# Performance work log

Measured on AMD Instinct MI355X. Metric: run time of the kernel, lower is better.

The kernel has to match this reference:

```python
import jax, jax.numpy as jnp
import numpy as np

N = 100000
D = 256
E = 300000


def setup_inputs() -> dict:
    key = jax.random.key(0)
    ks = jax.random.split(key, 9)
    x_all = jax.random.normal(ks[0], (N, D), dtype=jnp.float32)
    edge_index = jax.random.randint(ks[1], (2, E), 0, N, dtype=jnp.int64)
    s = 1.0 / np.sqrt(D)
    params = {}
    for i, layer in enumerate(["1", "2", "3"]):
        params[f"Wl{layer}"] = jax.random.uniform(ks[2 + 2 * i], (D, D), jnp.float32, -s, s)
        params[f"Wr{layer}"] = jax.random.uniform(ks[3 + 2 * i], (D, D), jnp.float32, -s, s)
        params[f"b{layer}"] = jnp.zeros((D,), jnp.float32)
    return {"edge_index": edge_index, "x_all": x_all, **params}


def sage_conv(x, src, dst, Wl, Wr, b):
    # PyG SAGEConv: lin_l(mean_{j in N(i)} x_j) + lin_r(x_i), bias on lin_l
    msgs = x[src]                                        # [E, D] gather
    agg = jax.ops.segment_sum(msgs, dst, num_segments=N)  # [N, D]
    deg = jax.ops.segment_sum(jnp.ones((src.shape[0],), x.dtype), dst, num_segments=N)
    agg = agg / jnp.maximum(deg, 1.0)[:, None]           # mean; isolated nodes -> 0
    return agg @ Wl.T + x @ Wr.T + b


def reference(edge_index, x_all, Wl1, Wr1, b1, Wl2, Wr2, b2, Wl3, Wr3, b3):
    src, dst = edge_index[0], edge_index[1]
    x = jax.nn.relu(sage_conv(x_all, src, dst, Wl1, Wr1, b1))
    # dropout p=0.4 is identity at inference (training=False)
    x = jax.nn.relu(sage_conv(x, src, dst, Wl2, Wr2, b2))
    x = sage_conv(x, src, dst, Wl3, Wr3, b3)
    return x
```

## Files before the change

### kernel.cpp

```cpp
#include <hip/hip_runtime.h>

typedef unsigned short ushort_t;
typedef unsigned int   u32;
typedef __attribute__((ext_vector_type(8))) short bf16x8;
typedef __attribute__((ext_vector_type(4))) float f32x4;

#define NNODES 100000
#define DIM    256
#define NEDGE  300000
#define KSTEPS 16
#define BROWS  64
#define SLICE  16384
#define MFMA16 __builtin_amdgcn_mfma_f32_16x16x32_bf16


__global__ void count_kernel(const int* __restrict__ dst, int* __restrict__ cnt, int E) {
    int e = blockIdx.x * blockDim.x + threadIdx.x;
    if (e < E) atomicAdd(&cnt[dst[e]], 1);
}

__global__ void scan1(const int* __restrict__ cnt, int* __restrict__ partial, int n) {
    __shared__ int s[256];
    int i = blockIdx.x * 256 + threadIdx.x;
    s[threadIdx.x] = (i < n) ? cnt[i] : 0;
    __syncthreads();
    for (int off = 128; off > 0; off >>= 1) {
        if (threadIdx.x < off) s[threadIdx.x] += s[threadIdx.x + off];
        __syncthreads();
    }
    if (threadIdx.x == 0) partial[blockIdx.x] = s[0];
}

__global__ void scan2(int* __restrict__ partial, int nb) {
    __shared__ int s[512];
    int t = threadIdx.x;
    int orig = (t < nb) ? partial[t] : 0;
    s[t] = orig;
    __syncthreads();
    for (int off = 1; off < 512; off <<= 1) {
        int v = (t >= off) ? s[t - off] : 0;
        __syncthreads();
        s[t] += v;
        __syncthreads();
    }
    if (t < nb) partial[t] = s[t] - orig;
}

__global__ void scan3(const int* __restrict__ cnt, const int* __restrict__ partial,
                      int* __restrict__ row_start, int n) {
    __shared__ int s[256];
    int i = blockIdx.x * 256 + threadIdx.x;
    int v = (i < n) ? cnt[i] : 0;
    s[threadIdx.x] = v;
    __syncthreads();
    for (int off = 1; off < 256; off <<= 1) {
        int t = (threadIdx.x >= off) ? s[threadIdx.x - off] : 0;
        __syncthreads();
        s[threadIdx.x] += t;
        __syncthreads();
    }
    if (i < n) row_start[i] = partial[blockIdx.x] + s[threadIdx.x] - v;
}

__global__ void fill_csr(const int* __restrict__ src, const int* __restrict__ dst,
                         const int* __restrict__ row_start, int* __restrict__ cursor,
                         int* __restrict__ esrc, int E) {
    int e = blockIdx.x * blockDim.x + threadIdx.x;
    if (e < E) {
        int d = dst[e];
        int pos = row_start[d] + atomicAdd(&cursor[d], 1);
        esrc[pos] = src[e];
    }
}


__device__ __forceinline__ float bfhi(unsigned u) { return __uint_as_float(u << 16); }
__device__ __forceinline__ float bflo(unsigned u) { return __uint_as_float(u & 0xFFFF0000u); }

__device__ __forceinline__ void split4pack(float v0, float v1, float v2, float v3,
                                           uint2& hi, uint2& lo) {
    unsigned u0 = __float_as_uint(v0), u1 = __float_as_uint(v1);
    unsigned u2 = __float_as_uint(v2), u3 = __float_as_uint(v3);
    hi.x = (u0 >> 16) | (u1 & 0xFFFF0000u);
    hi.y = (u2 >> 16) | (u3 & 0xFFFF0000u);
    unsigned w0 = __float_as_uint(v0 - bflo(u0)), w1 = __float_as_uint(v1 - bflo(u1));
    unsigned w2 = __float_as_uint(v2 - bflo(u2)), w3 = __float_as_uint(v3 - bflo(u3));
    lo.x = (w0 >> 16) | (w1 & 0xFFFF0000u);
    lo.y = (w2 >> 16) | (w3 & 0xFFFF0000u);
}

__global__ __launch_bounds__(256) void split_x(const float* __restrict__ x,
                                               ushort_t* __restrict__ x2) {
    int idx = blockIdx.x * 256 + threadIdx.x;
    if (idx >= NNODES * 64) return;
    int node = idx >> 6, lane = idx & 63;
    float4 v = ((const float4*)(x + (size_t)node * DIM))[lane];
    uint2 hi, lo;
    split4pack(v.x, v.y, v.z, v.w, hi, lo);
    *(uint2*)(x2 + (size_t)node * 512 + lane * 4)       = hi;
    *(uint2*)(x2 + (size_t)node * 512 + 256 + lane * 4) = lo;
}

__global__ __launch_bounds__(256) void aggregate2(
    const int* __restrict__ esrc, const int* __restrict__ row_start,
    const int* __restrict__ cnt, const ushort_t* __restrict__ x2,
    ushort_t* __restrict__ agg2)
{
    int node = (blockIdx.x * blockDim.x + threadIdx.x) >> 6;
    int lane = threadIdx.x & 63;
    if (node >= NNODES) return;
    int start = row_start[node];
    int c = cnt[node];
    float a0 = 0.f, a1 = 0.f, a2 = 0.f, a3 = 0.f;
    for (int i = 0; i < c; i++) {
        int s = esrc[start + i];
        const uint2 h = *(const uint2*)(x2 + (size_t)s * 512 + lane * 4);
        const uint2 l = *(const uint2*)(x2 + (size_t)s * 512 + 256 + lane * 4);
        a0 += bfhi(h.x) + bfhi(l.x);
        a1 += bflo(h.x) + bflo(l.x);
        a2 += bfhi(h.y) + bfhi(l.y);
        a3 += bflo(h.y) + bflo(l.y);
    }
    float inv = (c > 0) ? 1.0f / (float)c : 0.0f;
    uint2 hi, lo;
    split4pack(a0 * inv, a1 * inv, a2 * inv, a3 * inv, hi, lo);
    *(uint2*)(agg2 + (size_t)node * 512 + lane * 4)       = hi;
    *(uint2*)(agg2 + (size_t)node * 512 + 256 + lane * 4) = lo;
}

__global__ void conv_weights(const float* __restrict__ Wl, const float* __restrict__ Wr,
                             ushort_t* __restrict__ Bsw) {
    int idx = blockIdx.x * 256 + threadIdx.x;
    if (idx >= 256 * 512) return;
    int n = idx >> 9, k = idx & 511;
    float v = (k < DIM) ? Wl[n * DIM + k] : Wr[n * DIM + (k - DIM)];
    unsigned u = __float_as_uint(v);
    float lo = v - bflo(u);
    int ks = k >> 5, q = (k >> 3) & 3, j = k & 7;
    int ct = n >> 4, nn = n & 15;
    int base = ks * SLICE + ct * 512 + q * 128 + nn * 8 + j;
    Bsw[base]        = (ushort_t)(u >> 16);
    Bsw[base + 8192] = (ushort_t)(__float_as_uint(lo) >> 16);
}

__global__ __launch_bounds__(256, 4) void sage_gemm_mfma(
    const ushort_t* __restrict__ agg2, const ushort_t* __restrict__ xin2,
    const ushort_t* __restrict__ Bsw, const float* __restrict__ bias,
    void* __restrict__ outp, int M, int out_split)
{
    const int tid  = threadIdx.x;
    const int lane = tid & 63;
    const int cg   = tid >> 6;
    const int lrow = lane & 15;
    const int quad = lane >> 4;

    const int rowbase = blockIdx.x * BROWS;
    int r[4];
    #pragma unroll
    for (int rt = 0; rt < 4; rt++)
        r[rt] = min(rowbase + rt * 16 + lrow, M - 1);
    const int kq = quad * 8;
    const int ctbase = cg * 4;

    f32x4 acc[4][4];
    #pragma unroll
    for (int i = 0; i < 4; i++)
        #pragma unroll
        for (int j = 0; j < 4; j++)
            acc[i][j] = (f32x4){0.f, 0.f, 0.f, 0.f};

    #pragma unroll
    for (int ks = 0; ks < KSTEPS; ks++) {
        const ushort_t* ab = (ks < 8) ? agg2 : xin2;
        const int kk = (ks & 7) * 32 + kq;

        bf16x8 fh[4], fl[4];
        #pragma unroll
        for (int rt = 0; rt < 4; rt++) {
            const ushort_t* p = ab + (size_t)r[rt] * 512 + kk;
            fh[rt] = *(const bf16x8*)(p);
            fl[rt] = *(const bf16x8*)(p + 256);
        }

        const ushort_t* bp = Bsw + (size_t)ks * SLICE + ctbase * 512 + lane * 8;

        __builtin_amdgcn_s_setprio(1);
        #pragma unroll
        for (int ct = 0; ct < 4; ct++) {
            const bf16x8 bh = *(const bf16x8*)(bp + ct * 512);
            const bf16x8 bl = *(const bf16x8*)(bp + 8192 + ct * 512);
            #pragma unroll
            for (int rt = 0; rt < 4; rt++) {
                acc[rt][ct] = MFMA16(fh[rt], bh, acc[rt][ct], 0, 0, 0);
                acc[rt][ct] = MFMA16(fl[rt], bh, acc[rt][ct], 0, 0, 0);
                acc[rt][ct] = MFMA16(fh[rt], bl, acc[rt][ct], 0, 0, 0);
            }
        }
        __builtin_amdgcn_s_setprio(0);
    }

    __syncthreads();

    #pragma unroll
    for (int ct = 0; ct < 4; ct++) {
        const int col = (ctbase + ct) * 16 + lrow;
        const float bv = bias[col];
        #pragma unroll
        for (int rt = 0; rt < 4; rt++) {
            const int row = rowbase + rt * 16 + quad * 4;
            #pragma unroll
            for (int rr = 0; rr < 4; rr++) {
                if (row + rr < M) {
                    float v = acc[rt][ct][rr] + bv;
                    if (out_split) {
                        v = fmaxf(v, 0.f);
                        unsigned u = __float_as_uint(v);
                        float lo = v - bflo(u);
                        ushort_t* o = (ushort_t*)outp + (size_t)(row + rr) * 512 + col;
                        o[0]   = (ushort_t)(u >> 16);
                        o[256] = (ushort_t)(__float_as_uint(lo) >> 16);
                    } else {
                        ((float*)outp)[(size_t)(row + rr) * DIM + col] = v;
                    }
                }
            }
        }
    }
}

extern "C" void kernel_launch(void* const* d_in, const int* in_sizes, int n_in,
                              void* d_out, int out_size, void* d_ws, size_t ws_size,
                              hipStream_t stream) {
    const int*   edge = (const int*)d_in[0];
    const int*   src  = edge;
    const int*   dst  = edge + NEDGE;
    const float* x    = (const float*)d_in[1];
    const float* Wl1  = (const float*)d_in[2];
    const float* Wr1  = (const float*)d_in[3];
    const float* b1   = (const float*)d_in[4];
    const float* Wl2  = (const float*)d_in[5];
    const float* Wr2  = (const float*)d_in[6];
    const float* b2   = (const float*)d_in[7];
    const float* Wl3  = (const float*)d_in[8];
    const float* Wr3  = (const float*)d_in[9];
    const float* b3   = (const float*)d_in[10];

    ushort_t* agg2      = (ushort_t*)d_ws;
    int*      cnt       = (int*)(agg2 + (size_t)NNODES * 512);
    int*      row_start = cnt + NNODES;
    int*      cursor    = row_start + NNODES;
    int*      partial   = cursor + NNODES;
    int*      esrc      = partial + 512;
    ushort_t* Bsw       = (ushort_t*)(esrc + NEDGE);

    ushort_t* x2 = (ushort_t*)d_out;

    const int nScanBlocks = (NNODES + 255) / 256;

    hipMemsetAsync(cnt, 0, NNODES * sizeof(int), stream);
    hipMemsetAsync(cursor, 0, NNODES * sizeof(int), stream);
    count_kernel<<<(NEDGE + 255) / 256, 256, 0, stream>>>(dst, cnt, NEDGE);
    scan1<<<nScanBlocks, 256, 0, stream>>>(cnt, partial, NNODES);
    scan2<<<1, 512, 0, stream>>>(partial, nScanBlocks);
    scan3<<<nScanBlocks, 256, 0, stream>>>(cnt, partial, row_start, NNODES);
    fill_csr<<<(NEDGE + 255) / 256, 256, 0, stream>>>(src, dst, row_start, cursor, esrc, NEDGE);

    split_x<<<(NNODES * 64 + 255) / 256, 256, 0, stream>>>(x, x2);

    const int aggBlocks  = (NNODES * 64 + 255) / 256;
    const int gemmBlocks = (NNODES + BROWS - 1) / BROWS;
    const int convBlocks = (256 * 512 + 255) / 256;

    conv_weights<<<convBlocks, 256, 0, stream>>>(Wl1, Wr1, Bsw);
    aggregate2<<<aggBlocks, 256, 0, stream>>>(esrc, row_start, cnt, x2, agg2);
    sage_gemm_mfma<<<gemmBlocks, 256, 0, stream>>>(agg2, x2, Bsw, b1, (void*)x2, NNODES, 1);

    conv_weights<<<convBlocks, 256, 0, stream>>>(Wl2, Wr2, Bsw);
    aggregate2<<<aggBlocks, 256, 0, stream>>>(esrc, row_start, cnt, x2, agg2);
    sage_gemm_mfma<<<gemmBlocks, 256, 0, stream>>>(agg2, x2, Bsw, b2, (void*)x2, NNODES, 1);

    conv_weights<<<convBlocks, 256, 0, stream>>>(Wl3, Wr3, Bsw);
    aggregate2<<<aggBlocks, 256, 0, stream>>>(esrc, row_start, cnt, x2, agg2);
    sage_gemm_mfma<<<gemmBlocks, 256, 0, stream>>>(agg2, x2, Bsw, b3, d_out, NNODES, 0);
}
```

Before: 760.9 us.

## Stage weight column slice in LDS and split GEMM across column blocks

The GEMM is restructured so each 512-thread block covers 512 rows and one 64-column slice of the output. That slice's weight panel (64K bf16 halves) is loaded into LDS once per block via global_load_lds, instead of every wave reading B from global memory each k-step. A-fragments are double-buffered with a two-step register prefetch. Because output is now written by four independent column blocks, the in-place output buffer is replaced with rotating R1/R2/R3 buffers to avoid read-after-write hazards. In exchange, each A row is now read by four blocks and the kernel uses 128KB of LDS per block.

```diff
diff --git a/kernel.cpp b/kernel.cpp
--- a/kernel.cpp
+++ b/kernel.cpp
@@ -9,8 +9,9 @@
 #define DIM    256
 #define NEDGE  300000
 #define KSTEPS 16
-#define BROWS  64
-#define SLICE  16384
+#define BROWS  512
+#define CCOLS  64
+#define CREG   65536
 #define MFMA16 __builtin_amdgcn_mfma_f32_16x16x32_bf16
 
 
@@ -136,31 +137,46 @@
     float v = (k < DIM) ? Wl[n * DIM + k] : Wr[n * DIM + (k - DIM)];
     unsigned u = __float_as_uint(v);
     float lo = v - bflo(u);
+    int cb = n >> 6, ct = (n >> 4) & 3, nn = n & 15;
     int ks = k >> 5, q = (k >> 3) & 3, j = k & 7;
-    int ct = n >> 4, nn = n & 15;
-    int base = ks * SLICE + ct * 512 + q * 128 + nn * 8 + j;
+    int base = cb * CREG + ks * 4096 + ct * 512 + q * 128 + nn * 8 + j;
     Bsw[base]        = (ushort_t)(u >> 16);
-    Bsw[base + 8192] = (ushort_t)(__float_as_uint(lo) >> 16);
-}
-
-__global__ __launch_bounds__(256, 4) void sage_gemm_mfma(
-    const ushort_t* __restrict__ agg2, const ushort_t* __restrict__ xin2,
+    Bsw[base + 2048] = (ushort_t)(__float_as_uint(lo) >> 16);
+}
+
+__global__ __launch_bounds__(512, 2) void sage_gemm_mfma(
+    const ushort_t* __restrict__ aggp, const ushort_t* __restrict__ xinp,
     const ushort_t* __restrict__ Bsw, const float* __restrict__ bias,
     void* __restrict__ outp, int M, int out_split)
 {
+    __shared__ __align__(16) ushort_t Bs[CREG];
+
     const int tid  = threadIdx.x;
     const int lane = tid & 63;
-    const int cg   = tid >> 6;
+    const int wave = tid >> 6;
     const int lrow = lane & 15;
     const int quad = lane >> 4;
 
-    const int rowbase = blockIdx.x * BROWS;
+    const int rb = blockIdx.x >> 2;
+    const int cb = blockIdx.x & 3;
+
+    const int rowbase = rb * BROWS + wave * 64;
     int r[4];
     #pragma unroll
     for (int rt = 0; rt < 4; rt++)
         r[rt] = min(rowbase + rt * 16 + lrow, M - 1);
     const int kq = quad * 8;
-    const int ctbase = cg * 4;
+
+    const ushort_t* breg = Bsw + (size_t)cb * CREG;
+    #pragma unroll
+    for (int i = 0; i < 16; i++) {
+        const int c      = tid + i * 512;
+        const int cbase  = wave * 64 + i * 512;
+        __builtin_amdgcn_global_load_lds(
+            (const __attribute__((address_space(1))) u32*)(breg + (size_t)c * 8),
+            (__attribute__((address_space(3))) u32*)(Bs + cbase * 8),
+            16, 0, 0);
+    }
 
     f32x4 acc[4][4];
     #pragma unroll
@@ -169,58 +185,69 @@
         for (int j = 0; j < 4; j++)
             acc[i][j] = (f32x4){0.f, 0.f, 0.f, 0.f};
 
+    bf16x8 fr[2][8];
+    #pragma unroll
+    for (int rt = 0; rt < 4; rt++) {
+        const ushort_t* p = aggp + (size_t)r[rt] * 512 + kq;
+        fr[0][2 * rt]     = *(const bf16x8*)(p);
+        fr[0][2 * rt + 1] = *(const bf16x8*)(p + 256);
+        const ushort_t* q2 = aggp + (size_t)r[rt] * 512 + 32 + kq;
+        fr[1][2 * rt]     = *(const bf16x8*)(q2);
+        fr[1][2 * rt + 1] = *(const bf16x8*)(q2 + 256);
+    }
+
+    __syncthreads();
+
     #pragma unroll
     for (int ks = 0; ks < KSTEPS; ks++) {
-        const ushort_t* ab = (ks < 8) ? agg2 : xin2;
-        const int kk = (ks & 7) * 32 + kq;
-
-        bf16x8 fh[4], fl[4];
-        #pragma unroll
-        for (int rt = 0; rt < 4; rt++) {
-            const ushort_t* p = ab + (size_t)r[rt] * 512 + kk;
-            fh[rt] = *(const bf16x8*)(p);
-            fl[rt] = *(const bf16x8*)(p + 256);
-        }
-
-        const ushort_t* bp = Bsw + (size_t)ks * SLICE + ctbase * 512 + lane * 8;
-
-        __builtin_amdgcn_s_setprio(1);
+        const ushort_t* bp = Bs + ks * 4096 + lane * 8;
         #pragma unroll
         for (int ct = 0; ct < 4; ct++) {
             const bf16x8 bh = *(const bf16x8*)(bp + ct * 512);
-            const bf16x8 bl = *(const bf16x8*)(bp + 8192 + ct * 512);
+            const bf16x8 bl = *(const bf16x8*)(bp + 2048 + ct * 512);
             #pragma unroll
             for (int rt = 0; rt < 4; rt++) {
-                acc[rt][ct] = MFMA16(fh[rt], bh, acc[rt][ct], 0, 0, 0);
-                acc[rt][ct] = MFMA16(fl[rt], bh, acc[rt][ct], 0, 0, 0);
-                acc[rt][ct] = MFMA16(fh[rt], bl, acc[rt][ct], 0, 0, 0);
+                acc[rt][ct] = MFMA16(fr[ks & 1][2 * rt],     bh, acc[rt][ct], 0, 0, 0);
+                acc[rt][ct] = MFMA16(fr[ks & 1][2 * rt + 1], bh, acc[rt][ct], 0, 0, 0);
+                acc[rt][ct] = MFMA16(fr[ks & 1][2 * rt],     bl, acc[rt][ct], 0, 0, 0);
             }
         }
-        __builtin_amdgcn_s_setprio(0);
-    }
-
-    __syncthreads();
-
-    #pragma unroll
-    for (int ct = 0; ct < 4; ct++) {
-        const int col = (ctbase + ct) * 16 + lrow;
-        const float bv = bias[col];
+        if (ks + 2 < KSTEPS) {
+            const int k2 = ks + 2;
+            const ushort_t* ab = (k2 < 8) ? aggp : xinp;
+            const int kk = (k2 & 7) * 32 + kq;
+            #pragma unroll
+            for (int rt = 0; rt < 4; rt++) {
+                const ushort_t* p = ab + (size_t)r[rt] * 512 + kk;
+                fr[ks & 1][2 * rt]     = *(const bf16x8*)(p);
+                fr[ks & 1][2 * rt + 1] = *(const bf16x8*)(p + 256);
+            }
+        }
+    }
+
+    #pragma unroll
+    for (int rt = 0; rt < 4; rt++) {
         #pragma unroll
-        for (int rt = 0; rt < 4; rt++) {
-            const int row = rowbase + rt * 16 + quad * 4;
-            #pragma unroll
-            for (int rr = 0; rr < 4; rr++) {
-                if (row + rr < M) {
-                    float v = acc[rt][ct][rr] + bv;
-                    if (out_split) {
-                        v = fmaxf(v, 0.f);
+        for (int rr = 0; rr < 4; rr++) {
+            const int row = rowbase + rt * 16 + quad * 4 + rr;
+            if (row < M) {
+                if (out_split) {
+                    ushort_t* orow = (ushort_t*)outp + (size_t)row * 512;
+                    #pragma unroll
+                    for (int ct = 0; ct < 4; ct++) {
+                        const int col = cb * CCOLS + ct * 16 + lrow;
+                        float v = fmaxf(acc[rt][ct][rr] + bias[col], 0.f);
                         unsigned u = __float_as_uint(v);
                         float lo = v - bflo(u);
-                        ushort_t* o = (ushort_t*)outp + (size_t)(row + rr) * 512 + col;
-                        o[0]   = (ushort_t)(u >> 16);
-                        o[256] = (ushort_t)(__float_as_uint(lo) >> 16);
-                    } else {
-                        ((float*)outp)[(size_t)(row + rr) * DIM + col] = v;
+                        orow[col]       = (ushort_t)(u >> 16);
+                        orow[col + 256] = (ushort_t)(__float_as_uint(lo) >> 16);
+                    }
+                } else {
+                    float* orow = (float*)outp + (size_t)row * DIM;
+                    #pragma unroll
+                    for (int ct = 0; ct < 4; ct++) {
+                        const int col = cb * CCOLS + ct * 16 + lrow;
+                        orow[col] = acc[rt][ct][rr] + bias[col];
                     }
                 }
             }
@@ -245,15 +272,17 @@
     const float* Wr3  = (const float*)d_in[9];
     const float* b3   = (const float*)d_in[10];
 
-    ushort_t* agg2      = (ushort_t*)d_ws;
-    int*      cnt       = (int*)(agg2 + (size_t)NNODES * 512);
+    const size_t feat = (size_t)NNODES * 512;
+
+    ushort_t* R1        = (ushort_t*)d_ws;
+    ushort_t* R2        = R1 + feat;
+    int*      cnt       = (int*)(R2 + feat);
     int*      row_start = cnt + NNODES;
     int*      cursor    = row_start + NNODES;
     int*      partial   = cursor + NNODES;
     int*      esrc      = partial + 512;
     ushort_t* Bsw       = (ushort_t*)(esrc + NEDGE);
-
-    ushort_t* x2 = (ushort_t*)d_out;
+    ushort_t* R3        = (ushort_t*)d_out;
 
     const int nScanBlocks = (NNODES + 255) / 256;
 
@@ -265,21 +294,21 @@
     scan3<<<nScanBlocks, 256, 0, stream>>>(cnt, partial, row_start, NNODES);
     fill_csr<<<(NEDGE + 255) / 256, 256, 0, stream>>>(src, dst, row_start, cursor, esrc, NEDGE);
 
-    split_x<<<(NNODES * 64 + 255) / 256, 256, 0, stream>>>(x, x2);
+    split_x<<<(NNODES * 64 + 255) / 256, 256, 0, stream>>>(x, R1);
 
     const int aggBlocks  = (NNODES * 64 + 255) / 256;
-    const int gemmBlocks = (NNODES + BROWS - 1) / BROWS;
+    const int gemmBlocks = ((NNODES + BROWS - 1) / BROWS) * 4;
     const int convBlocks = (256 * 512 + 255) / 256;
 
     conv_weights<<<convBlocks, 256, 0, stream>>>(Wl1, Wr1, Bsw);
-    aggregate2<<<aggBlocks, 256, 0, stream>>>(esrc, row_start, cnt, x2, agg2);
-    sage_gemm_mfma<<<gemmBlocks, 256, 0, stream>>>(agg2, x2, Bsw, b1, (void*)x2, NNODES, 1);
+    aggregate2<<<aggBlocks, 256, 0, stream>>>(esrc, row_start, cnt, R1, R2);
+    sage_gemm_mfma<<<gemmBlocks, 512, 0, stream>>>(R2, R1, Bsw, b1, (void*)R3, NNODES, 1);
 
     conv_weights<<<convBlocks, 256, 0, stream>>>(Wl2, Wr2, Bsw);
-    aggregate2<<<aggBlocks, 256, 0, stream>>>(esrc, row_start, cnt, x2, agg2);
-    sage_gemm_mfma<<<gemmBlocks, 256, 0, stream>>>(agg2, x2, Bsw, b2, (void*)x2, NNODES, 1);
+    aggregate2<<<aggBlocks, 256, 0, stream>>>(esrc, row_start, cnt, R3, R1);
+    sage_gemm_mfma<<<gemmBlocks, 512, 0, stream>>>(R1, R3, Bsw, b2, (void*)R2, NNODES, 1);
 
     conv_weights<<<convBlocks, 256, 0, stream>>>(Wl3, Wr3, Bsw);
-    aggregate2<<<aggBlocks, 256, 0, stream>>>(esrc, row_start, cnt, x2, agg2);
-    sage_gemm_mfma<<<gemmBlocks, 256, 0, stream>>>(agg2, x2, Bsw, b3, d_out, NNODES, 0);
-}
+    aggregate2<<<aggBlocks, 256, 0, stream>>>(esrc, row_start, cnt, R2, R1);
+    sage_gemm_mfma<<<gemmBlocks, 512, 0, stream>>>(R1, R2, Bsw, b3, d_out, NNODES, 0);
+}
```

Result: slower. 834.8 us (+9.7%).
